# Performance work log

Measured on AMD Instinct MI355X. Metric: run time of the kernel, lower is better.

Reference implementation:

```python
import jax, jax.numpy as jnp
import numpy as np

N_NODES = 20000
N_EDGES = 640000
N_TRIP = 1000000
C = 128          # channels
E = 64           # expansion_features
CUTOFF = 5.0
LOG2 = float(np.log(2.0))


def ssp(x):
    # ShiftedSoftplus
    return jax.nn.softplus(x) - LOG2


def setup_inputs() -> dict:
    key = jax.random.key(0)
    ks = jax.random.split(key, 12)
    features = jax.random.normal(ks[0], (N_NODES, C), dtype=jnp.float32)
    neighbour_distances = jax.random.uniform(ks[1], (N_EDGES,), dtype=jnp.float32) * (1.2 * CUTOFF)
    neighbour_list = jax.random.randint(ks[2], (2, N_EDGES), 0, N_NODES, dtype=jnp.int32)
    triplet_idxs = jax.random.randint(ks[3], (N_TRIP, 3), 0, N_NODES, dtype=jnp.int32)
    angles = jax.random.uniform(ks[4], (N_TRIP,), dtype=jnp.float32) * np.pi
    r_ij = jax.random.uniform(ks[5], (N_TRIP,), dtype=jnp.float32) * CUTOFF
    r_ik = jax.random.uniform(ks[6], (N_TRIP,), dtype=jnp.float32) * CUTOFF
    # learned parameters (Linear layers without bias; stored [in, out])
    W_pre = jax.random.normal(ks[7], (C, C), dtype=jnp.float32) / np.sqrt(C)
    W2b1 = jax.random.normal(ks[8], (E, E), dtype=jnp.float32) / np.sqrt(E)
    W2b2 = jax.random.normal(ks[9], (E, C), dtype=jnp.float32) / np.sqrt(E)
    W3b1 = jax.random.normal(ks[10], (3, C // 2), dtype=jnp.float32) / np.sqrt(3.0)
    W3b2 = jax.random.normal(ks[11], (C // 2, C), dtype=jnp.float32) / np.sqrt(C // 2)
    W_post = jax.random.normal(jax.random.fold_in(key, 99), (C, C), dtype=jnp.float32) / np.sqrt(C)
    return {
        "features": features,
        "neighbour_distances": neighbour_distances,
        "neighbour_list": neighbour_list,
        "triplet_idxs": triplet_idxs,
        "angles": angles,
        "r_ij": r_ij,
        "r_ik": r_ik,
        "W_pre": W_pre,
        "W2b1": W2b1,
        "W2b2": W2b2,
        "W3b1": W3b1,
        "W3b2": W3b2,
        "W_post": W_post,
    }


def reference(features, neighbour_distances, neighbour_list, triplet_idxs,
              angles, r_ij, r_ik, W_pre, W2b1, W2b2, W3b1, W3b2, W_post):
    # 1) pre-linear
    h = features @ W_pre                                   # [N, C]

    # 2) radial basis (Gaussian smearing) with smooth cosine cutoff envelope
    centers = jnp.linspace(0.0, CUTOFF, E, dtype=jnp.float32)  # [E]
    width = CUTOFF / E
    gamma = 1.0 / (2.0 * width * width)
    d = neighbour_distances[:, None]                       # [n_edges, 1]
    rb = jnp.exp(-gamma * (d - centers) ** 2)              # [n_edges, E]
    cutoff_mask = (neighbour_distances < CUTOFF).astype(jnp.float32)
    cutoff_values = 0.5 * (1.0 + jnp.cos(np.pi * neighbour_distances / CUTOFF))
    rb = rb * (cutoff_values * cutoff_mask)[:, None]       # fused envelope

    # 3) two-body messages: gather neighbour node features, modulate by radial MLP
    neighbor_h = h[neighbour_list[1]]                      # [n_edges, C]
    two_body = neighbor_h * (ssp(rb @ W2b1) @ W2b2)        # [n_edges, C]

    # 4) three-body messages: angular MLP on (r_ij, r_ik, cos(angle)),
    #    gather node features at triplet_idxs[:,1], scatter-add into edge slots
    tbf = jnp.stack([r_ij, r_ik, jnp.cos(angles)], axis=-1)  # [n_trip, 3]
    w3 = ssp(tbf @ W3b1) @ W3b2                              # [n_trip, C]
    msgs = h[triplet_idxs[:, 1]] * w3                        # [n_trip, C]
    edge_msgs = jnp.zeros_like(two_body).at[triplet_idxs[:, 1]].add(msgs)

    # 5) aggregate messages over neighbours (to central atom = neighbour_list[0])
    messages = two_body + edge_msgs
    agg = jax.ops.segment_sum(messages, neighbour_list[0], num_segments=N_NODES)

    # 6) post-linear
    return agg @ W_post
```

## Files before the change

kernel.cpp:

```cpp
#include <hip/hip_runtime.h>
#include <hip/hip_fp16.h>
#include <math.h>

#define TID threadIdx.x

typedef ushort u16x8 __attribute__((ext_vector_type(8)));
typedef unsigned char uchar;

static constexpr int NN = 20000;
static constexpr int NE = 640000;
static constexpr int NT = 1000000;
static constexpr int C = 128;
static constexpr int E = 64;
static constexpr int LUTN = 4104;
static constexpr int NBKT = 313;
static constexpr int NB2 = 512;
static constexpr int CHE2 = 1250;
static constexpr int CHT2 = 1954;
static constexpr float CUT = 5.0f;
static constexpr float LN2 = 0.69314718055994530942f;

__device__ __forceinline__ float ssp(float x) {
    return fmaxf(x, 0.0f) + __logf(1.0f + __expf(-fabsf(x))) - LN2;
}

__device__ __forceinline__ float sp_raw(float x) {
    return fmaxf(x, 0.0f) + __logf(1.0f + __expf(-fabsf(x)));
}

__device__ __forceinline__ ushort f2bf(float x) {
    uint u = __float_as_uint(x);
    return (ushort)((u + 0x7FFFu + ((u >> 16) & 1u)) >> 16);
}

__device__ __forceinline__ float bf2f(ushort u) {
    return __uint_as_float((uint)u << 16);
}

__device__ __forceinline__ float h2f(uint bits) {
    return __half2float(__ushort_as_half((ushort)(bits & 0xFFFFu)));
}

__global__ __launch_bounds__(256) void k_gemm16f(const float* __restrict__ A,
                                                 const float* __restrict__ W,
                                                 float* __restrict__ out, int nrows) {
    __shared__ ushort wB[C * C];
    __shared__ float aL[16][132];
    for (int i = TID; i < C * C / 4; i += 256) {
        float4 w4 = ((const float4*)W)[i];
        ushort4 u = {f2bf(w4.x), f2bf(w4.y), f2bf(w4.z), f2bf(w4.w)};
        ((ushort4*)wB)[i] = u;
    }
    const int base = blockIdx.x * 16;
    for (int i = TID; i < 512; i += 256) {
        int r = base + (i >> 5);
        float4 v = (r < nrows) ? ((const float4*)A)[(size_t)r * 32 + (i & 31)]
                               : (float4){0.f, 0.f, 0.f, 0.f};
        *(float4*)&aL[i >> 5][(i & 31) << 2] = v;
    }
    __syncthreads();
    const int rg = TID >> 4;
    const int c8 = (TID & 15) << 3;
    float acc[8] = {0.f, 0.f, 0.f, 0.f, 0.f, 0.f, 0.f, 0.f};
    #pragma unroll 8
    for (int k = 0; k < C; ++k) {
        float a = aL[rg][k];
        u16x8 wv = *(const u16x8*)&wB[k * C + c8];
        #pragma unroll
        for (int j = 0; j < 8; ++j) acc[j] = fmaf(a, bf2f(wv[j]), acc[j]);
    }
    int r = base + rg;
    if (r < nrows) {
        float4 o0 = {acc[0], acc[1], acc[2], acc[3]};
        float4 o1 = {acc[4], acc[5], acc[6], acc[7]};
        *(float4*)&out[(size_t)r * C + c8] = o0;
        *(float4*)&out[(size_t)r * C + c8 + 4] = o1;
    }
}

__global__ __launch_bounds__(256) void k_gemm16b(const float* __restrict__ A,
                                                 const float* __restrict__ W,
                                                 ushort* __restrict__ outB, int nrows) {
    __shared__ ushort wB[C * C];
    __shared__ float aL[16][132];
    for (int i = TID; i < C * C / 4; i += 256) {
        float4 w4 = ((const float4*)W)[i];
        ushort4 u = {f2bf(w4.x), f2bf(w4.y), f2bf(w4.z), f2bf(w4.w)};
        ((ushort4*)wB)[i] = u;
    }
    const int base = blockIdx.x * 16;
    for (int i = TID; i < 512; i += 256) {
        int r = base + (i >> 5);
        float4 v = (r < nrows) ? ((const float4*)A)[(size_t)r * 32 + (i & 31)]
                               : (float4){0.f, 0.f, 0.f, 0.f};
        *(float4*)&aL[i >> 5][(i & 31) << 2] = v;
    }
    __syncthreads();
    const int rg = TID >> 4;
    const int c8 = (TID & 15) << 3;
    float acc[8] = {0.f, 0.f, 0.f, 0.f, 0.f, 0.f, 0.f, 0.f};
    #pragma unroll 8
    for (int k = 0; k < C; ++k) {
        float a = aL[rg][k];
        u16x8 wv = *(const u16x8*)&wB[k * C + c8];
        #pragma unroll
        for (int j = 0; j < 8; ++j) acc[j] = fmaf(a, bf2f(wv[j]), acc[j]);
    }
    int r = base + rg;
    if (r < nrows) {
        u16x8 u;
        #pragma unroll
        for (int j = 0; j < 8; ++j) u[j] = f2bf(acc[j]);
        *(u16x8*)&outB[(size_t)r * C + c8] = u;
    }
}

__global__ __launch_bounds__(256) void k_lut(const float* __restrict__ W2b1,
                                             const float* __restrict__ W2b2,
                                             ushort* __restrict__ lutB) {
    __shared__ float w1[E * E];
    __shared__ float w2[E * C];
    __shared__ float rbL[8][E];
    __shared__ float hid[8][E];
    for (int i = TID; i < E * E; i += 256) w1[i] = W2b1[i];
    for (int i = TID; i < E * C; i += 256) w2[i] = W2b2[i];
    const int jj = TID & 63;
    const int esA = TID >> 6;
    const int eg = TID >> 5;
    const int c4 = (TID & 31) << 2;
    const float gamma = 81.92f;
    const float cstep = CUT / 63.0f;
    const float delta = CUT / 4096.0f;
    const int base = blockIdx.x * 8;
    __syncthreads();
    #pragma unroll
    for (int s = 0; s < 2; ++s) {
        int es = esA + 4 * s;
        float d = (float)(base + es) * delta;
        float cv = (d < CUT) ? 0.5f * (1.0f + __cosf((float)M_PI * d / CUT)) : 0.0f;
        float dd = d - (float)jj * cstep;
        rbL[es][jj] = __expf(-gamma * dd * dd) * cv;
    }
    __syncthreads();
    #pragma unroll
    for (int s = 0; s < 2; ++s) {
        int es = esA + 4 * s;
        float a = 0.f;
        #pragma unroll 16
        for (int k = 0; k < E; ++k)
            a = fmaf(rbL[es][k], w1[k * E + jj], a);
        hid[es][jj] = ssp(a);
    }
    __syncthreads();
    float4 o = {0.f, 0.f, 0.f, 0.f};
    #pragma unroll
    for (int j = 0; j < E; ++j) {
        float t = hid[eg][j];
        const float4 w4 = *(const float4*)&w2[j * C + c4];
        o.x = fmaf(t, w4.x, o.x);
        o.y = fmaf(t, w4.y, o.y);
        o.z = fmaf(t, w4.z, o.z);
        o.w = fmaf(t, w4.w, o.w);
    }
    int row = base + eg;
    if (row < LUTN) {
        ushort4 u = {f2bf(o.x), f2bf(o.y), f2bf(o.z), f2bf(o.w)};
        *(ushort4*)&lutB[(size_t)row * C + c4] = u;
    }
}

__global__ __launch_bounds__(256) void k_bcount(const int* __restrict__ nl0,
                                                const int* __restrict__ tidx,
                                                uchar* __restrict__ cntE,
                                                uchar* __restrict__ cntT) {
    __shared__ int h[NBKT];
    const int b = blockIdx.x;
    for (int i = TID; i < NBKT; i += 256) h[i] = 0;
    __syncthreads();
    const int e0 = b * CHE2, e1 = min(e0 + CHE2, NE);
    for (int i = e0 + TID; i < e1; i += 256) atomicAdd(&h[nl0[i] >> 6], 1);
    __syncthreads();
    for (int i = TID; i < NBKT; i += 256) { cntE[(size_t)i * NB2 + b] = (uchar)h[i]; h[i] = 0; }
    __syncthreads();
    const int t0 = b * CHT2, t1 = min(t0 + CHT2, NT);
    for (int i = t0 + TID; i < t1; i += 256) atomicAdd(&h[tidx[3 * i + 1] >> 6], 1);
    __syncthreads();
    for (int i = TID; i < NBKT; i += 256) cntT[(size_t)i * NB2 + b] = (uchar)h[i];
}

__global__ __launch_bounds__(256) void k_bscan(const uchar* __restrict__ cE,
                                               const uchar* __restrict__ cT,
                                               ushort* __restrict__ baseE,
                                               ushort* __restrict__ baseT,
                                               int* __restrict__ totEb,
                                               int* __restrict__ totTb) {
    const int lane = TID & 63;
    const int wv = TID >> 6;
    int task = blockIdx.x * 4 + wv;
    if (task >= 2 * NBKT) return;
    const bool isE = task < NBKT;
    const int k = isE ? task : task - NBKT;
    const uchar* src = isE ? cE : cT;
    ushort* dst = isE ? baseE : baseT;
    int* dT = isE ? totEb : totTb;
    int v[8], pre[8], s = 0;
    #pragma unroll
    for (int j = 0; j < 8; ++j) {
        v[j] = src[(size_t)k * NB2 + lane * 8 + j];
        pre[j] = s;
        s += v[j];
    }
    int incl = s;
    #pragma unroll
    for (int off = 1; off < 64; off <<= 1) {
        int t = __shfl_up(incl, off, 64);
        if (lane >= off) incl += t;
    }
    int excl = incl - s;
    #pragma unroll
    for (int j = 0; j < 8; ++j)
        dst[(size_t)k * NB2 + lane * 8 + j] = (ushort)(excl + pre[j]);
    if (lane == 63) dT[k] = incl;
}

__device__ void scan_one(const int* __restrict__ hist, int* __restrict__ start, int n) {
    __shared__ int wsum[16];
    __shared__ int carryS;
    const int lane = TID & 63;
    const int wv = TID >> 6;
    if (TID == 0) carryS = 0;
    __syncthreads();
    for (int base = 0; base < n; base += 1024) {
        int i = base + TID;
        int v = (i < n) ? hist[i] : 0;
        int acc = v;
        #pragma unroll
        for (int off = 1; off < 64; off <<= 1) {
            int t = __shfl_up(acc, off, 64);
            if (lane >= off) acc += t;
        }
        if (lane == 63) wsum[wv] = acc;
        __syncthreads();
        int woff = 0;
        for (int w = 0; w < wv; ++w) woff += wsum[w];
        int excl = carryS + woff + acc - v;
        if (i < n) start[i] = excl;
        __syncthreads();
        if (TID == 1023) carryS = excl + v;
        __syncthreads();
    }
}

__global__ __launch_bounds__(1024) void k_bktscan(const int* __restrict__ totEb, int* __restrict__ bksE,
                                                  const int* __restrict__ totTb, int* __restrict__ bksT) {
    if (blockIdx.x == 0) scan_one(totEb, bksE, NBKT);
    else                 scan_one(totTb, bksT, NBKT);
}

__global__ __launch_bounds__(256) void k_bplace(const int* __restrict__ nl0,
                                                const int* __restrict__ nl1,
                                                const float* __restrict__ dist,
                                                const int* __restrict__ tidx,
                                                const float* __restrict__ angles,
                                                const float* __restrict__ rij,
                                                const float* __restrict__ rik,
                                                const ushort* __restrict__ baseE,
                                                const ushort* __restrict__ baseT,
                                                const int* __restrict__ bksE,
                                                const int* __restrict__ bksT,
                                                int2* __restrict__ eT,
                                                int2* __restrict__ tT) {
    __shared__ int cur[NBKT];
    const int b = blockIdx.x;
    for (int k = TID; k < NBKT; k += 256)
        cur[k] = bksE[k] + (int)baseE[(size_t)k * NB2 + b];
    __syncthreads();
    const int e0 = b * CHE2, e1 = min(e0 + CHE2, NE);
    for (int i = e0 + TID; i < e1; i += 256) {
        int n0 = nl0[i];
        int pos = atomicAdd(&cur[n0 >> 6], 1);
        uint tq = (uint)fmaf(dist[i], 209715.2f, 0.5f);
        eT[pos] = make_int2((int)(tq | ((uint)(n0 & 63) << 26)), nl1[i]);
    }
    __syncthreads();
    for (int k = TID; k < NBKT; k += 256)
        cur[k] = bksT[k] + (int)baseT[(size_t)k * NB2 + b];
    __syncthreads();
    const int t0 = b * CHT2, tEnd = min(t0 + CHT2, NT);
    for (int i = t0 + TID; i < tEnd; i += 256) {
        int t1 = tidx[3 * i + 1];
        int pos = atomicAdd(&cur[t1 >> 6], 1);
        uint ab = ((uint)__half_as_ushort(__float2half_rn(rik[i])) << 16)
                | (uint)__half_as_ushort(__float2half_rn(rij[i]));
        uint cc = (uint)__half_as_ushort(__float2half_rn(__cosf(angles[i])))
                | ((uint)(t1 & 63) << 16);
        tT[pos] = make_int2((int)ab, (int)cc);
    }
}

__global__ __launch_bounds__(256) void k_nsort(const int2* __restrict__ eTs,
                                               const int2* __restrict__ tTs,
                                               const int* __restrict__ bksE,
                                               const int* __restrict__ bksT,
                                               const int* __restrict__ totEb,
                                               const int* __restrict__ totTb,
                                               int2* __restrict__ eS,
                                               int2* __restrict__ tS,
                                               int* __restrict__ startE,
                                               int* __restrict__ totE,
                                               int* __restrict__ startT,
                                               int* __restrict__ totT) {
    __shared__ int hist[64];
    __shared__ int cur[64];
    const bool isE = blockIdx.x < NBKT;
    const int bkt = isE ? blockIdx.x : blockIdx.x - NBKT;
    const int2* src = isE ? eTs : tTs;
    int2* dst = isE ? eS : tS;
    const int s0 = isE ? bksE[bkt] : bksT[bkt];
    const int cnt = isE ? totEb[bkt] : totTb[bkt];
    int* stX = isE ? startE : startT;
    int* ttX = isE ? totE : totT;
    if (TID < 64) hist[TID] = 0;
    __syncthreads();
    for (int i = TID; i < cnt; i += 256) {
        int2 p = src[s0 + i];
        int nlo = isE ? (int)(((uint)p.x >> 26) & 63u) : (int)(((uint)p.y >> 16) & 63u);
        atomicAdd(&hist[nlo], 1);
    }
    __syncthreads();
    if (TID < 64) {
        int v = hist[TID];
        int incl = v;
        #pragma unroll
        for (int off = 1; off < 64; off <<= 1) {
            int t = __shfl_up(incl, off, 64);
            if (TID >= off) incl += t;
        }
        int excl = incl - v;
        cur[TID] = s0 + excl;
        int node = bkt * 64 + TID;
        if (node < NN) { stX[node] = s0 + excl; ttX[node] = v; }
    }
    __syncthreads();
    for (int i = TID; i < cnt; i += 256) {
        int2 p = src[s0 + i];
        int nlo = isE ? (int)(((uint)p.x >> 26) & 63u) : (int)(((uint)p.y >> 16) & 63u);
        int pos = atomicAdd(&cur[nlo], 1);
        dst[pos] = p;
    }
}

__global__ __launch_bounds__(256) void k_edges_node(const int2* __restrict__ eS,
                                                    const int* __restrict__ startE,
                                                    const int* __restrict__ totE,
                                                    const ushort* __restrict__ hB,
                                                    const ushort* __restrict__ lutB,
                                                    float* __restrict__ agg) {
    __shared__ int2 stage[4][64];
    const int lane = TID & 63;
    const int wv = TID >> 6;
    const int c2 = lane << 1;
    for (int r = blockIdx.x * 4 + wv; r < NN; r += gridDim.x * 4) {
        const int s0 = startE[r];
        const int cnt = totE[r];
        float a0 = 0.f, a1 = 0.f;
        for (int base = 0; base < cnt; base += 64) {
            const int n = min(64, cnt - base);
            if (lane < n) stage[wv][lane] = eS[s0 + base + lane];
            asm volatile("s_waitcnt lgkmcnt(0)" ::: "memory");
            #pragma unroll 4
            for (int i = 0; i < n; ++i) {
                int2 p = stage[wv][i];
                uint tq = ((uint)p.x) & 0x03FFFFFFu;
                int n1 = p.y;
                int idx = min((int)(tq >> 8), LUTN - 2);
                float fr = (float)(tq & 255u) * (1.0f / 256.0f);
                ushort2 A2 = *(const ushort2*)&lutB[(size_t)idx * C + c2];
                ushort2 B2 = *(const ushort2*)&lutB[(size_t)(idx + 1) * C + c2];
                ushort2 H2 = *(const ushort2*)&hB[(size_t)n1 * C + c2];
                float ax = bf2f(A2.x), ay = bf2f(A2.y);
                float ox = fmaf(fr, bf2f(B2.x) - ax, ax);
                float oy = fmaf(fr, bf2f(B2.y) - ay, ay);
                a0 = fmaf(ox, bf2f(H2.x), a0);
                a1 = fmaf(oy, bf2f(H2.y), a1);
            }
            asm volatile("s_waitcnt lgkmcnt(0)" ::: "memory");
        }
        float2 o = {a0, a1};
        *(float2*)&agg[(size_t)r * C + c2] = o;
    }
}

__global__ __launch_bounds__(256) void k_trip_node(const int* __restrict__ startT,
                                                   const int* __restrict__ totT,
                                                   const int2* __restrict__ tS,
                                                   const float* __restrict__ W3b1,
                                                   const float* __restrict__ W3b2,
                                                   const ushort* __restrict__ hB,
                                                   const int* __restrict__ nl0,
                                                   float* __restrict__ agg) {
    __shared__ float w2[64 * C];
    __shared__ uint2 stage[4][64];
    for (int i = TID; i < 64 * C; i += 256) w2[i] = W3b2[i];
    __syncthreads();
    const int lane = TID & 63;
    const int wv = TID >> 6;
    const float w1a = W3b1[lane];
    const float w1b = W3b1[64 + lane];
    const float w1c = W3b1[128 + lane];
    for (int r = blockIdx.x * 4 + wv; r < NN; r += gridDim.x * 4) {
        const int s0 = startT[r];
        const int cnt = totT[r];
        float usum = 0.f;
        for (int base = 0; base < cnt; base += 64) {
            const int n = min(64, cnt - base);
            if (lane < n)
                stage[wv][lane] = ((const uint2*)tS)[s0 + base + lane];
            asm volatile("s_waitcnt lgkmcnt(0)" ::: "memory");
            #pragma unroll 4
            for (int i = 0; i < n; ++i) {
                uint2 p = stage[wv][i];
                float ri = h2f(p.x);
                float rk = h2f(p.x >> 16);
                float ca = h2f(p.y);
                float x = fmaf(ri, w1a, fmaf(rk, w1b, ca * w1c));
                usum += sp_raw(x);
            }
            asm volatile("s_waitcnt lgkmcnt(0)" ::: "memory");
        }
        usum -= LN2 * (float)cnt;
        float o0 = 0.f, o1 = 0.f;
        #pragma unroll 8
        for (int k = 0; k < 64; ++k) {
            float uk = __shfl(usum, k, 64);
            o0 = fmaf(uk, w2[k * C + lane], o0);
            o1 = fmaf(uk, w2[k * C + 64 + lane], o1);
        }
        const int n0 = nl0[r];
        float h0 = bf2f(hB[(size_t)r * C + lane]);
        float h1 = bf2f(hB[(size_t)r * C + 64 + lane]);
        unsafeAtomicAdd(&agg[(size_t)n0 * C + lane], o0 * h0);
        unsafeAtomicAdd(&agg[(size_t)n0 * C + 64 + lane], o1 * h1);
    }
}

extern "C" void kernel_launch(void* const* d_in, const int* in_sizes, int n_in,
                              void* d_out, int out_size, void* d_ws, size_t ws_size,
                              hipStream_t stream) {
    const float* features = (const float*)d_in[0];
    const float* ndist    = (const float*)d_in[1];
    const int*   nlist    = (const int*)d_in[2];
    const int*   tidx     = (const int*)d_in[3];
    const float* angles   = (const float*)d_in[4];
    const float* rij      = (const float*)d_in[5];
    const float* rik      = (const float*)d_in[6];
    const float* W_pre    = (const float*)d_in[7];
    const float* W2b1     = (const float*)d_in[8];
    const float* W2b2     = (const float*)d_in[9];
    const float* W3b1     = (const float*)d_in[10];
    const float* W3b2     = (const float*)d_in[11];
    const float* W_post   = (const float*)d_in[12];
    float* out = (float*)d_out;

    char* w = (char*)d_ws;
    float* agg    = (float*)w;
    int2* eT      = (int2*)w;
    w += (size_t)NN * C * 4;
    ushort* hB    = (ushort*)w;  w += (size_t)NN * C * 2;
    ushort* lutB  = (ushort*)w;  w += (size_t)LUTN * C * 2;
    int2* eS      = (int2*)w;    w += (size_t)NE * 8;
    int2* tS      = (int2*)w;    w += (size_t)NT * 8;
    int2* tT      = (int2*)w;    w += (size_t)NT * 8;
    uchar* cntE   = (uchar*)w;   w += (size_t)NBKT * NB2;
    uchar* cntT   = (uchar*)w;   w += (size_t)NBKT * NB2;
    ushort* baseE = (ushort*)w;  w += (size_t)NBKT * NB2 * 2;
    ushort* baseT = (ushort*)w;  w += (size_t)NBKT * NB2 * 2;
    int* totEb    = (int*)w;     w += 1280;
    int* totTb    = (int*)w;     w += 1280;
    int* bksE     = (int*)w;     w += 1280;
    int* bksT     = (int*)w;     w += 1280;
    int* startE   = (int*)w;     w += (size_t)NN * 4;
    int* totE     = (int*)w;     w += (size_t)NN * 4;
    int* startT   = (int*)w;     w += (size_t)NN * 4;
    int* totT     = (int*)w;     w += (size_t)NN * 4;

    const int* nl0 = nlist;
    const int* nl1 = nlist + NE;

    hipLaunchKernelGGL(k_gemm16b, dim3((NN + 15) / 16), dim3(256), 0, stream,
                       features, W_pre, hB, NN);
    hipLaunchKernelGGL(k_lut, dim3((LUTN + 7) / 8), dim3(256), 0, stream,
                       W2b1, W2b2, lutB);
    hipLaunchKernelGGL(k_bcount, dim3(NB2), dim3(256), 0, stream,
                       nl0, tidx, cntE, cntT);
    hipLaunchKernelGGL(k_bscan, dim3((2 * NBKT + 3) / 4), dim3(256), 0, stream,
                       cntE, cntT, baseE, baseT, totEb, totTb);
    hipLaunchKernelGGL(k_bktscan, dim3(2), dim3(1024), 0, stream,
                       totEb, bksE, totTb, bksT);
    hipLaunchKernelGGL(k_bplace, dim3(NB2), dim3(256), 0, stream,
                       nl0, nl1, ndist, tidx, angles, rij, rik,
                       baseE, baseT, bksE, bksT, eT, tT);
    hipLaunchKernelGGL(k_nsort, dim3(2 * NBKT), dim3(256), 0, stream,
                       eT, tT, bksE, bksT, totEb, totTb,
                       eS, tS, startE, totE, startT, totT);
    hipLaunchKernelGGL(k_edges_node, dim3(2500), dim3(256), 0, stream,
                       eS, startE, totE, hB, lutB, agg);
    hipLaunchKernelGGL(k_trip_node, dim3(2500), dim3(256), 0, stream,
                       startT, totT, tS, W3b1, W3b2, hB, nl0, agg);
    hipLaunchKernelGGL(k_gemm16f, dim3((NN + 15) / 16), dim3(256), 0, stream,
                       agg, W_post, out, NN);
}
```

Before: 194.1 us.

## Replace softplus transcendentals with LUT, precompute edge offsets, bf16-pack angular weights

The triplet kernel replaces the per-triplet exp/log softplus with a 512-entry linearly interpolated table of log1p(exp(-|x|)), which an extra block of the LUT kernel builds into shared memory. Half-precision decoding moves into the cooperative staging step so the inner loop reads ready floats. The W3b2 weights are packed as bf16 pairs to halve shared memory, and the edge kernel stages precomputed byte offsets and fractions per edge instead of recomputing them in every lane. The aim is to cut transcendental and integer work in the hot loops, at the cost of approximation error from the table (inputs beyond |x|=16 are clamped) and bf16 weights.

After: 192.0 us. About the same (-1.0%).

```diff
diff --git a/kernel.cpp b/kernel.cpp
--- a/kernel.cpp
+++ b/kernel.cpp
@@ -24,10 +24,6 @@
     return fmaxf(x, 0.0f) + __logf(1.0f + __expf(-fabsf(x))) - LN2;
 }
 
-__device__ __forceinline__ float sp_raw(float x) {
-    return fmaxf(x, 0.0f) + __logf(1.0f + __expf(-fabsf(x)));
-}
-
 __device__ __forceinline__ ushort f2bf(float x) {
     uint u = __float_as_uint(x);
     return (ushort)((u + 0x7FFFu + ((u >> 16) & 1u)) >> 16);
@@ -117,7 +113,18 @@
 
 __global__ __launch_bounds__(256) void k_lut(const float* __restrict__ W2b1,
                                              const float* __restrict__ W2b2,
-                                             ushort* __restrict__ lutB) {
+                                             ushort* __restrict__ lutB,
+                                             float2* __restrict__ spLut) {
+    if (blockIdx.x == (LUTN + 7) / 8) {
+        for (int e = TID; e < 512; e += 256) {
+            float t0 = (float)e * (1.0f / 32.0f);
+            float t1 = (float)(e + 1) * (1.0f / 32.0f);
+            float v0 = log1pf(__expf(-t0));
+            float v1 = log1pf(__expf(-t1));
+            spLut[e] = make_float2(v0, v1 - v0);
+        }
+        return;
+    }
     __shared__ float w1[E * E];
     __shared__ float w2[E * C];
     __shared__ float rbL[8][E];
@@ -356,28 +363,32 @@
                                                     const ushort* __restrict__ hB,
                                                     const ushort* __restrict__ lutB,
                                                     float* __restrict__ agg) {
-    __shared__ int2 stage[4][64];
+    __shared__ int4 stage[4][64];
     const int lane = TID & 63;
     const int wv = TID >> 6;
-    const int c2 = lane << 1;
+    const int c2b = lane << 2;
     for (int r = blockIdx.x * 4 + wv; r < NN; r += gridDim.x * 4) {
         const int s0 = startE[r];
         const int cnt = totE[r];
         float a0 = 0.f, a1 = 0.f;
         for (int base = 0; base < cnt; base += 64) {
             const int n = min(64, cnt - base);
-            if (lane < n) stage[wv][lane] = eS[s0 + base + lane];
-            asm volatile("s_waitcnt lgkmcnt(0)" ::: "memory");
-            #pragma unroll 4
-            for (int i = 0; i < n; ++i) {
-                int2 p = stage[wv][i];
+            if (lane < n) {
+                int2 p = eS[s0 + base + lane];
                 uint tq = ((uint)p.x) & 0x03FFFFFFu;
-                int n1 = p.y;
                 int idx = min((int)(tq >> 8), LUTN - 2);
                 float fr = (float)(tq & 255u) * (1.0f / 256.0f);
-                ushort2 A2 = *(const ushort2*)&lutB[(size_t)idx * C + c2];
-                ushort2 B2 = *(const ushort2*)&lutB[(size_t)(idx + 1) * C + c2];
-                ushort2 H2 = *(const ushort2*)&hB[(size_t)n1 * C + c2];
+                stage[wv][lane] = make_int4(idx * (C * 2), __float_as_int(fr),
+                                            p.y * (C * 2), 0);
+            }
+            asm volatile("s_waitcnt lgkmcnt(0)" ::: "memory");
+            #pragma unroll 8
+            for (int i = 0; i < n; ++i) {
+                int4 q = stage[wv][i];
+                float fr = __int_as_float(q.y);
+                ushort2 A2 = *(const ushort2*)((const char*)lutB + q.x + c2b);
+                ushort2 B2 = *(const ushort2*)((const char*)lutB + q.x + 256 + c2b);
+                ushort2 H2 = *(const ushort2*)((const char*)hB + q.z + c2b);
                 float ax = bf2f(A2.x), ay = bf2f(A2.y);
                 float ox = fmaf(fr, bf2f(B2.x) - ax, ax);
                 float oy = fmaf(fr, bf2f(B2.y) - ay, ay);
@@ -387,7 +398,7 @@
             asm volatile("s_waitcnt lgkmcnt(0)" ::: "memory");
         }
         float2 o = {a0, a1};
-        *(float2*)&agg[(size_t)r * C + c2] = o;
+        *(float2*)&agg[(size_t)r * C + (lane << 1)] = o;
     }
 }
 
@@ -396,12 +407,20 @@
                                                    const int2* __restrict__ tS,
                                                    const float* __restrict__ W3b1,
                                                    const float* __restrict__ W3b2,
+                                                   const float2* __restrict__ spLut,
                                                    const ushort* __restrict__ hB,
                                                    const int* __restrict__ nl0,
                                                    float* __restrict__ agg) {
-    __shared__ float w2[64 * C];
-    __shared__ uint2 stage[4][64];
-    for (int i = TID; i < 64 * C; i += 256) w2[i] = W3b2[i];
+    __shared__ uint w2p[64 * 64];
+    __shared__ float2 spl[512];
+    __shared__ float4 stage[4][64];
+    for (int i = TID; i < 512; i += 256) spl[i] = spLut[i];
+    for (int i = TID; i < 4096; i += 256) {
+        int k = i >> 6, l = i & 63;
+        float lo = W3b2[k * C + l];
+        float hi = W3b2[k * C + 64 + l];
+        w2p[i] = ((uint)f2bf(hi) << 16) | (uint)f2bf(lo);
+    }
     __syncthreads();
     const int lane = TID & 63;
     const int wv = TID >> 6;
@@ -414,17 +433,25 @@
         float usum = 0.f;
         for (int base = 0; base < cnt; base += 64) {
             const int n = min(64, cnt - base);
-            if (lane < n)
-                stage[wv][lane] = ((const uint2*)tS)[s0 + base + lane];
+            if (lane < n) {
+                uint2 p = ((const uint2*)tS)[s0 + base + lane];
+                float4 f;
+                f.x = h2f(p.x);
+                f.y = h2f(p.x >> 16);
+                f.z = h2f(p.y);
+                f.w = 0.f;
+                stage[wv][lane] = f;
+            }
             asm volatile("s_waitcnt lgkmcnt(0)" ::: "memory");
             #pragma unroll 4
             for (int i = 0; i < n; ++i) {
-                uint2 p = stage[wv][i];
-                float ri = h2f(p.x);
-                float rk = h2f(p.x >> 16);
-                float ca = h2f(p.y);
-                float x = fmaf(ri, w1a, fmaf(rk, w1b, ca * w1c));
-                usum += sp_raw(x);
+                float4 p = stage[wv][i];
+                float x = fmaf(p.x, w1a, fmaf(p.y, w1b, p.z * w1c));
+                float t = fabsf(x) * 32.0f;
+                int idx = min((int)t, 511);
+                float fr = t - (float)idx;
+                float2 vs = spl[idx];
+                usum += fmaxf(x, 0.f) + fmaf(fr, vs.y, vs.x);
             }
             asm volatile("s_waitcnt lgkmcnt(0)" ::: "memory");
         }
@@ -433,8 +460,11 @@
         #pragma unroll 8
         for (int k = 0; k < 64; ++k) {
             float uk = __shfl(usum, k, 64);
-            o0 = fmaf(uk, w2[k * C + lane], o0);
-            o1 = fmaf(uk, w2[k * C + 64 + lane], o1);
+            uint wp = w2p[k * 64 + lane];
+            float lo = __uint_as_float(wp << 16);
+            float hi = __uint_as_float(wp & 0xFFFF0000u);
+            o0 = fmaf(uk, lo, o0);
+            o1 = fmaf(uk, hi, o1);
         }
         const int n0 = nl0[r];
         float h0 = bf2f(hB[(size_t)r * C + lane]);
@@ -483,14 +513,15 @@
     int* totE     = (int*)w;     w += (size_t)NN * 4;
     int* startT   = (int*)w;     w += (size_t)NN * 4;
     int* totT     = (int*)w;     w += (size_t)NN * 4;
+    float2* spLut = (float2*)w;  w += 512 * 8;
 
     const int* nl0 = nlist;
     const int* nl1 = nlist + NE;
 
     hipLaunchKernelGGL(k_gemm16b, dim3((NN + 15) / 16), dim3(256), 0, stream,
                        features, W_pre, hB, NN);
-    hipLaunchKernelGGL(k_lut, dim3((LUTN + 7) / 8), dim3(256), 0, stream,
-                       W2b1, W2b2, lutB);
+    hipLaunchKernelGGL(k_lut, dim3((LUTN + 7) / 8 + 1), dim3(256), 0, stream,
+                       W2b1, W2b2, lutB, spLut);
     hipLaunchKernelGGL(k_bcount, dim3(NB2), dim3(256), 0, stream,
                        nl0, tidx, cntE, cntT);
     hipLaunchKernelGGL(k_bscan, dim3((2 * NBKT + 3) / 4), dim3(256), 0, stream,
@@ -506,7 +537,7 @@
     hipLaunchKernelGGL(k_edges_node, dim3(2500), dim3(256), 0, stream,
                        eS, startE, totE, hB, lutB, agg);
     hipLaunchKernelGGL(k_trip_node, dim3(2500), dim3(256), 0, stream,
-                       startT, totT, tS, W3b1, W3b2, hB, nl0, agg);
+                       startT, totT, tS, W3b1, W3b2, spLut, hB, nl0, agg);
     hipLaunchKernelGGL(k_gemm16f, dim3((NN + 15) / 16), dim3(256), 0, stream,
                        agg, W_post, out, NN);
 }
```
